# Optimization experiments

Hardware: AMD Instinct MI355X
Metric: run time of the kernel (lower is better)

## Reference

```python
import jax, jax.numpy as jnp
import numpy as np
from jax import lax

REG_STRENGTH = 0.01
TEMPERATURE = 0.1


def _pav_nonincreasing(y):
    """Pool-adjacent-violators for isotonic L2 regression with a
    nonincreasing constraint (matches torchsort's isotonic_l2).
    Returns (solution [n], block_id [n])."""
    n = y.shape[0]

    def body(carry, yi):
        m, c, t = carry  # block means, block counts, stack top
        m = m.at[t].set(yi)
        c = c.at[t].set(1)

        def cond(st):
            m_, c_, t_ = st
            return (t_ > 0) & (m_[t_ - 1] < m_[t_])

        def merge(st):
            m_, c_, t_ = st
            tot = m_[t_ - 1] * c_[t_ - 1] + m_[t_] * c_[t_]
            cc = c_[t_ - 1] + c_[t_]
            m_ = m_.at[t_ - 1].set(tot / cc)
            c_ = c_.at[t_ - 1].set(cc).at[t_].set(0)
            return (m_, c_, t_ - 1)

        m, c, t = lax.while_loop(cond, merge, (m, c, t))
        return (m, c, t + 1), None

    init = (jnp.zeros(n, y.dtype), jnp.zeros(n, jnp.int32), jnp.int32(0))
    (m, c, _), _ = lax.scan(body, init, y)
    sol = jnp.repeat(m, c, total_repeat_length=n)
    blk = jnp.repeat(jnp.arange(n), c, total_repeat_length=n)
    return sol, blk


@jax.custom_vjp
def _isotonic_l2(y):
    return _pav_nonincreasing(y)[0]


def _iso_fwd(y):
    sol, blk = _pav_nonincreasing(y)
    return sol, blk


def _iso_bwd(blk, g):
    n = g.shape[0]
    sums = jax.ops.segment_sum(g, blk, num_segments=n)
    cnts = jax.ops.segment_sum(jnp.ones_like(g), blk, num_segments=n)
    return ((sums / jnp.maximum(cnts, 1.0))[blk],)


_isotonic_l2.defvjp(_iso_fwd, _iso_bwd)


def soft_sort_ascending(scores, reg_strength):
    """torchsort.soft_sort with L2 regularization. scores: [B, R]."""
    n = scores.shape[-1]
    w = jnp.arange(n, 0, -1, dtype=scores.dtype) / reg_strength  # [n, ..., 1]/rs
    perm = jnp.argsort(scores, axis=-1)
    s = -jnp.take_along_axis(scores, perm, axis=-1)  # descending sort of -scores
    sol = jax.vmap(_isotonic_l2)(w[None, :] - s)
    return sol - w  # ascending soft-sorted values, [B, R]


def setup_inputs() -> dict:
    key = jax.random.key(0)
    k1, k2 = jax.random.split(key)
    scores = jax.random.normal(k1, (128, 8192), dtype=jnp.float32)
    ref_class = jax.random.randint(k2, (8192,), 0, 10, dtype=jnp.int32)
    return {"scores": scores, "ref_class": ref_class, "k": 32, "K": 8}


def reference(scores, ref_class, k, K):
    B, R = scores.shape
    rc = ref_class
    if rc.ndim == 1:
        rc = jnp.broadcast_to(rc[None, :], (B, R))
    rc = rc.astype(scores.dtype)
    sorted_vals = soft_sort_ascending(scores, REG_STRENGTH)  # [B, R]
    yk = sorted_vals[:, -k:]                                  # top-k largest, [B, k]
    M = jnp.abs(scores[:, None, :] - yk[:, :, None])          # [B, k, R]
    soft_mask = jax.nn.softmax(-M / TEMPERATURE, axis=-1)     # [B, k, R]
    soft_label_expectation = jnp.einsum('bkr,br->bk', soft_mask, rc)
    return yk, soft_label_expectation
```

## Files before the change

kernel.cpp:

```cpp
#include <hip/hip_runtime.h>
#include <math.h>

#define R_N    8192
#define K_TOP  32
#define HALF_R 4096
#define NEG10_LOG2E (-14.426950408889634f)
#define CUT_DELTA   2.0f

__device__ __forceinline__ float fast_exp2(float x) {
#if __has_builtin(__builtin_amdgcn_exp2f)
    return __builtin_amdgcn_exp2f(x);
#else
    return exp2f(x);
#endif
}

__device__ __forceinline__ float merge_asc32(float v, int l) {
#pragma unroll
    for (int j = 16; j > 0; j >>= 1) {
        float pv = __shfl_xor(v, j, 64);
        v = ((l & j) == 0) ? fminf(v, pv) : fmaxf(v, pv);
    }
    return v;
}

__device__ __forceinline__ float sort32_asc(float v, int l) {
#pragma unroll
    for (int k = 2; k <= 32; k <<= 1) {
#pragma unroll
        for (int j = k >> 1; j > 0; j >>= 1) {
            float pv = __shfl_xor(v, j, 64);
            bool keep_min = (((l & k) == 0) == ((l & j) == 0));
            v = keep_min ? fminf(v, pv) : fmaxf(v, pv);
        }
    }
    return v;
}

__device__ __forceinline__ float merge_top32(float a, float b, int l) {
    float rev = __shfl_xor(b, 31, 64);
    return merge_asc32(fmaxf(a, rev), l);
}

extern "C" __global__ void __launch_bounds__(1024)
k_topk(const float* __restrict__ scores, float* __restrict__ out) {
    __shared__ float topbuf[32 * 32];
    const int row = blockIdx.x;
    const int tid = threadIdx.x;
    const int l   = tid & 31;
    const int h   = tid >> 5;

    const float4* s4 = (const float4*)(scores + (size_t)row * R_N);
    float4 a = s4[tid];
    float4 b = s4[tid + 1024];
    float v[8] = {a.x, a.y, a.z, a.w, b.x, b.y, b.z, b.w};

#pragma unroll
    for (int p = 0; p < 8; ++p) v[p] = sort32_asc(v[p], l);
#pragma unroll
    for (int gap = 1; gap < 8; gap <<= 1)
#pragma unroll
        for (int p = 0; p < 8; p += 2 * gap)
            v[p] = merge_top32(v[p], v[p + gap], l);
    float run = v[0];

#pragma unroll
    for (int stride = 1; stride < 32; stride <<= 1) {
        topbuf[h * 32 + l] = run;
        __syncthreads();
        if ((h & (2 * stride - 1)) == 0) {
            float pv = topbuf[(h + stride) * 32 + (l ^ 31)];
            run = merge_asc32(fmaxf(run, pv), l);
        }
        __syncthreads();
    }
    if (tid < 32) out[(size_t)row * K_TOP + l] = run;
}

extern "C" __global__ void __launch_bounds__(512)
k_expect(const float* __restrict__ scores, const int* __restrict__ rc,
         const float* __restrict__ yk, float* __restrict__ part) {
    __shared__ float2 comp[HALF_R];
    __shared__ float  yk_lds[K_TOP];
    __shared__ float  rnum[8][K_TOP >> 2][4];
    __shared__ unsigned int cnt;

    const int row  = blockIdx.x >> 1;
    const int half = blockIdx.x & 1;
    const int tid  = threadIdx.x;
    const int lane = tid & 63;
    const int wv   = tid >> 6;

    if (tid == 0) cnt = 0;
    if (tid < K_TOP) yk_lds[tid] = yk[(size_t)row * K_TOP + tid];
    __syncthreads();
    const float cutoff = yk_lds[0] - CUT_DELTA;

    const float4* s4 = (const float4*)(scores + (size_t)row * R_N + half * HALF_R);
    const int4*   c4 = (const int4*)(rc + half * HALF_R);
    float se[8], ce[8];
#pragma unroll
    for (int q = 0; q < 2; ++q) {
        float4 s = s4[tid + q * 512];
        int4   c = c4[tid + q * 512];
        se[q*4+0] = s.x; se[q*4+1] = s.y; se[q*4+2] = s.z; se[q*4+3] = s.w;
        ce[q*4+0] = (float)c.x; ce[q*4+1] = (float)c.y;
        ce[q*4+2] = (float)c.z; ce[q*4+3] = (float)c.w;
    }
#pragma unroll
    for (int e = 0; e < 8; ++e) {
        bool keep = (se[e] >= cutoff);
        unsigned long long m = __ballot(keep);
        unsigned int base = 0;
        if (lane == 0) base = atomicAdd(&cnt, (unsigned)__popcll(m));
        base = __shfl(base, 0, 64);
        if (keep) {
            unsigned int pre = (unsigned)__popcll(m & ((1ull << lane) - 1ull));
            comp[base + pre] = make_float2(se[e], ce[e]);
        }
    }
    __syncthreads();
    const int n = (int)cnt;

    const int j0 = wv * 4;
    const float y0 = yk_lds[j0 + 0], y1 = yk_lds[j0 + 1];
    const float y2 = yk_lds[j0 + 2], y3 = yk_lds[j0 + 3];
    float n0 = 0, d0 = 0, n1 = 0, d1 = 0, n2 = 0, d2 = 0, n3 = 0, d3 = 0;
    for (int i = lane; i < n; i += 64) {
        float2 p = comp[i];
        float e0 = fast_exp2(NEG10_LOG2E * fabsf(p.x - y0));
        float e1 = fast_exp2(NEG10_LOG2E * fabsf(p.x - y1));
        float e2 = fast_exp2(NEG10_LOG2E * fabsf(p.x - y2));
        float e3 = fast_exp2(NEG10_LOG2E * fabsf(p.x - y3));
        n0 = fmaf(e0, p.y, n0); d0 += e0;
        n1 = fmaf(e1, p.y, n1); d1 += e1;
        n2 = fmaf(e2, p.y, n2); d2 += e2;
        n3 = fmaf(e3, p.y, n3); d3 += e3;
    }
#pragma unroll
    for (int off = 32; off > 0; off >>= 1) {
        n0 += __shfl_xor(n0, off, 64); d0 += __shfl_xor(d0, off, 64);
        n1 += __shfl_xor(n1, off, 64); d1 += __shfl_xor(d1, off, 64);
        n2 += __shfl_xor(n2, off, 64); d2 += __shfl_xor(d2, off, 64);
        n3 += __shfl_xor(n3, off, 64); d3 += __shfl_xor(d3, off, 64);
    }
    if (lane == 0) {
        rnum[wv][0][0] = n0; rnum[wv][0][1] = n1;
        rnum[wv][0][2] = n2; rnum[wv][0][3] = n3;
    }
    if (lane == 1) {
        rnum[wv][1][0] = d0; rnum[wv][1][1] = d1;
        rnum[wv][1][2] = d2; rnum[wv][1][3] = d3;
    }
    __syncthreads();
    if (tid < 2 * K_TOP) {
        int which = tid >> 5;
        int j     = tid & 31;
        float v = rnum[j >> 2][which][j & 3];
        part[((size_t)row * 2 + half) * (2 * K_TOP) + which * K_TOP + j] = v;
    }
}

extern "C" __global__ void __launch_bounds__(256)
k_final(const float* __restrict__ part, float* __restrict__ out, int B) {
    const int g   = blockIdx.x * 256 + threadIdx.x;
    const int row = g >> 5;
    const int j   = g & 31;
    const float* p = part + (size_t)row * 2 * (2 * K_TOP);
    float num = p[j] + p[2 * K_TOP + j];
    float den = p[K_TOP + j] + p[3 * K_TOP + j];
    out[(size_t)B * K_TOP + g] = num / den;
}

extern "C" void kernel_launch(void* const* d_in, const int* in_sizes, int n_in,
                              void* d_out, int out_size, void* d_ws, size_t ws_size,
                              hipStream_t stream) {
    const float* scores = (const float*)d_in[0];
    const int*   rc     = (const int*)d_in[1];
    const int R = in_sizes[1];
    const int B = in_sizes[0] / R;
    float* out  = (float*)d_out;
    float* part = (float*)d_ws;

    hipLaunchKernelGGL(k_topk,   dim3(B),     dim3(1024), 0, stream, scores, out);
    hipLaunchKernelGGL(k_expect, dim3(B * 2), dim3(512),  0, stream, scores, rc, out, part);
    hipLaunchKernelGGL(k_final,  dim3((B * K_TOP) / 256), dim3(256), 0, stream, part, out, B);
}
```

Before: 75.98 us.

## Split top-k across half-row blocks, merge in expectation kernel, drop final kernel

The top-k kernel now runs two 512-thread blocks per row, each producing a partial top-32 into workspace. The expectation kernel uses one 1024-thread block per row: it merges the two partial top-32 lists, writes yk, compacts the candidate scores with one atomic per wave, and writes the final ratios directly. This removes the third launch and the partial-sum round trip. Class labels are stored as bytes in LDS, and each wave handles two top-k targets instead of four. The cost is that half as many blocks run the expectation stage, and each block uses larger LDS arrays.

```diff
diff --git a/kernel.cpp b/kernel.cpp
--- a/kernel.cpp
+++ b/kernel.cpp
@@ -42,17 +42,18 @@
     return merge_asc32(fmaxf(a, rev), l);
 }
 
-extern "C" __global__ void __launch_bounds__(1024)
-k_topk(const float* __restrict__ scores, float* __restrict__ out) {
-    __shared__ float topbuf[32 * 32];
-    const int row = blockIdx.x;
-    const int tid = threadIdx.x;
-    const int l   = tid & 31;
-    const int h   = tid >> 5;
+extern "C" __global__ void __launch_bounds__(512)
+k_topk(const float* __restrict__ scores, float* __restrict__ wstop) {
+    __shared__ float topbuf[16 * 32];
+    const int row  = blockIdx.x >> 1;
+    const int half = blockIdx.x & 1;
+    const int tid  = threadIdx.x;
+    const int l    = tid & 31;
+    const int h    = tid >> 5;
 
-    const float4* s4 = (const float4*)(scores + (size_t)row * R_N);
+    const float4* s4 = (const float4*)(scores + (size_t)row * R_N + half * HALF_R);
     float4 a = s4[tid];
-    float4 b = s4[tid + 1024];
+    float4 b = s4[tid + 512];
     float v[8] = {a.x, a.y, a.z, a.w, b.x, b.y, b.z, b.w};
 
 #pragma unroll
@@ -65,7 +66,7 @@
     float run = v[0];
 
 #pragma unroll
-    for (int stride = 1; stride < 32; stride <<= 1) {
+    for (int stride = 1; stride < 16; stride <<= 1) {
         topbuf[h * 32 + l] = run;
         __syncthreads();
         if ((h & (2 * stride - 1)) == 0) {
@@ -74,102 +75,90 @@
         }
         __syncthreads();
     }
-    if (tid < 32) out[(size_t)row * K_TOP + l] = run;
+    if (tid < 32) wstop[(size_t)blockIdx.x * K_TOP + l] = run;
 }
 
-extern "C" __global__ void __launch_bounds__(512)
+extern "C" __global__ void __launch_bounds__(1024)
 k_expect(const float* __restrict__ scores, const int* __restrict__ rc,
-         const float* __restrict__ yk, float* __restrict__ part) {
-    __shared__ float2 comp[HALF_R];
-    __shared__ float  yk_lds[K_TOP];
-    __shared__ float  rnum[8][K_TOP >> 2][4];
-    __shared__ unsigned int cnt;
+         const float* __restrict__ wstop, float* __restrict__ out, int B) {
+    __shared__ float         cs[R_N];
+    __shared__ unsigned char cc[R_N];
+    __shared__ float         yk_m[K_TOP];
+    __shared__ unsigned int  cnt;
 
-    const int row  = blockIdx.x >> 1;
-    const int half = blockIdx.x & 1;
+    const int row  = blockIdx.x;
     const int tid  = threadIdx.x;
     const int lane = tid & 63;
+    const int l    = tid & 31;
     const int wv   = tid >> 6;
 
     if (tid == 0) cnt = 0;
-    if (tid < K_TOP) yk_lds[tid] = yk[(size_t)row * K_TOP + tid];
-    __syncthreads();
-    const float cutoff = yk_lds[0] - CUT_DELTA;
 
-    const float4* s4 = (const float4*)(scores + (size_t)row * R_N + half * HALF_R);
-    const int4*   c4 = (const int4*)(rc + half * HALF_R);
-    float se[8], ce[8];
+    float A = wstop[(size_t)row * 2 * K_TOP + l];
+    float Bb = wstop[(size_t)row * 2 * K_TOP + K_TOP + l];
+    float run = merge_top32(A, Bb, l);
+    if (tid < K_TOP) {
+        yk_m[l] = run;
+        out[(size_t)row * K_TOP + l] = run;
+    }
+    const float cutoff = __shfl(run, 0, 64) - CUT_DELTA;
+
+    const float4* s4 = (const float4*)(scores + (size_t)row * R_N);
+    const int4*   c4 = (const int4*)rc;
+    float se[8]; int cei[8];
 #pragma unroll
     for (int q = 0; q < 2; ++q) {
-        float4 s = s4[tid + q * 512];
-        int4   c = c4[tid + q * 512];
+        float4 s = s4[tid + q * 1024];
+        int4   c = c4[tid + q * 1024];
         se[q*4+0] = s.x; se[q*4+1] = s.y; se[q*4+2] = s.z; se[q*4+3] = s.w;
-        ce[q*4+0] = (float)c.x; ce[q*4+1] = (float)c.y;
-        ce[q*4+2] = (float)c.z; ce[q*4+3] = (float)c.w;
+        cei[q*4+0] = c.x; cei[q*4+1] = c.y; cei[q*4+2] = c.z; cei[q*4+3] = c.w;
     }
+    __syncthreads();
+
+    unsigned long long m[8];
+    unsigned int tot = 0;
 #pragma unroll
     for (int e = 0; e < 8; ++e) {
-        bool keep = (se[e] >= cutoff);
-        unsigned long long m = __ballot(keep);
-        unsigned int base = 0;
-        if (lane == 0) base = atomicAdd(&cnt, (unsigned)__popcll(m));
-        base = __shfl(base, 0, 64);
-        if (keep) {
-            unsigned int pre = (unsigned)__popcll(m & ((1ull << lane) - 1ull));
-            comp[base + pre] = make_float2(se[e], ce[e]);
+        m[e] = __ballot(se[e] >= cutoff);
+        tot += (unsigned)__popcll(m[e]);
+    }
+    unsigned int wbase = 0;
+    if (lane == 0) wbase = atomicAdd(&cnt, tot);
+    wbase = __shfl(wbase, 0, 64);
+    const unsigned long long lt = (1ull << lane) - 1ull;
+#pragma unroll
+    for (int e = 0; e < 8; ++e) {
+        if (se[e] >= cutoff) {
+            unsigned int idx = wbase + (unsigned)__popcll(m[e] & lt);
+            cs[idx] = se[e];
+            cc[idx] = (unsigned char)cei[e];
         }
+        wbase += (unsigned)__popcll(m[e]);
     }
     __syncthreads();
     const int n = (int)cnt;
 
-    const int j0 = wv * 4;
-    const float y0 = yk_lds[j0 + 0], y1 = yk_lds[j0 + 1];
-    const float y2 = yk_lds[j0 + 2], y3 = yk_lds[j0 + 3];
-    float n0 = 0, d0 = 0, n1 = 0, d1 = 0, n2 = 0, d2 = 0, n3 = 0, d3 = 0;
+    const float y0 = yk_m[wv * 2 + 0];
+    const float y1 = yk_m[wv * 2 + 1];
+    float n0 = 0, d0 = 0, n1 = 0, d1 = 0;
     for (int i = lane; i < n; i += 64) {
-        float2 p = comp[i];
-        float e0 = fast_exp2(NEG10_LOG2E * fabsf(p.x - y0));
-        float e1 = fast_exp2(NEG10_LOG2E * fabsf(p.x - y1));
-        float e2 = fast_exp2(NEG10_LOG2E * fabsf(p.x - y2));
-        float e3 = fast_exp2(NEG10_LOG2E * fabsf(p.x - y3));
-        n0 = fmaf(e0, p.y, n0); d0 += e0;
-        n1 = fmaf(e1, p.y, n1); d1 += e1;
-        n2 = fmaf(e2, p.y, n2); d2 += e2;
-        n3 = fmaf(e3, p.y, n3); d3 += e3;
+        float s = cs[i];
+        float c = (float)cc[i];
+        float e0 = fast_exp2(NEG10_LOG2E * fabsf(s - y0));
+        float e1 = fast_exp2(NEG10_LOG2E * fabsf(s - y1));
+        n0 = fmaf(e0, c, n0); d0 += e0;
+        n1 = fmaf(e1, c, n1); d1 += e1;
     }
 #pragma unroll
     for (int off = 32; off > 0; off >>= 1) {
         n0 += __shfl_xor(n0, off, 64); d0 += __shfl_xor(d0, off, 64);
         n1 += __shfl_xor(n1, off, 64); d1 += __shfl_xor(d1, off, 64);
-        n2 += __shfl_xor(n2, off, 64); d2 += __shfl_xor(d2, off, 64);
-        n3 += __shfl_xor(n3, off, 64); d3 += __shfl_xor(d3, off, 64);
     }
     if (lane == 0) {
-        rnum[wv][0][0] = n0; rnum[wv][0][1] = n1;
-        rnum[wv][0][2] = n2; rnum[wv][0][3] = n3;
+        float* dst = out + (size_t)B * K_TOP + (size_t)row * K_TOP + wv * 2;
+        dst[0] = n0 / d0;
+        dst[1] = n1 / d1;
     }
-    if (lane == 1) {
-        rnum[wv][1][0] = d0; rnum[wv][1][1] = d1;
-        rnum[wv][1][2] = d2; rnum[wv][1][3] = d3;
-    }
-    __syncthreads();
-    if (tid < 2 * K_TOP) {
-        int which = tid >> 5;
-        int j     = tid & 31;
-        float v = rnum[j >> 2][which][j & 3];
-        part[((size_t)row * 2 + half) * (2 * K_TOP) + which * K_TOP + j] = v;
-    }
-}
-
-extern "C" __global__ void __launch_bounds__(256)
-k_final(const float* __restrict__ part, float* __restrict__ out, int B) {
-    const int g   = blockIdx.x * 256 + threadIdx.x;
-    const int row = g >> 5;
-    const int j   = g & 31;
-    const float* p = part + (size_t)row * 2 * (2 * K_TOP);
-    float num = p[j] + p[2 * K_TOP + j];
-    float den = p[K_TOP + j] + p[3 * K_TOP + j];
-    out[(size_t)B * K_TOP + g] = num / den;
 }
 
 extern "C" void kernel_launch(void* const* d_in, const int* in_sizes, int n_in,
@@ -179,10 +168,9 @@
     const int*   rc     = (const int*)d_in[1];
     const int R = in_sizes[1];
     const int B = in_sizes[0] / R;
-    float* out  = (float*)d_out;
-    float* part = (float*)d_ws;
+    float* out   = (float*)d_out;
+    float* wstop = (float*)d_ws;
 
-    hipLaunchKernelGGL(k_topk,   dim3(B),     dim3(1024), 0, stream, scores, out);
-    hipLaunchKernelGGL(k_expect, dim3(B * 2), dim3(512),  0, stream, scores, rc, out, part);
-    hipLaunchKernelGGL(k_final,  dim3((B * K_TOP) / 256), dim3(256), 0, stream, part, out, B);
+    hipLaunchKernelGGL(k_topk,   dim3(B * 2), dim3(512),  0, stream, scores, wstop);
+    hipLaunchKernelGGL(k_expect, dim3(B),     dim3(1024), 0, stream, scores, rc, wstop, out, B);
 }
```

After: 72.07 us. 5.2% less time.
